# Performance work log

Measured on AMD Instinct MI355X. Metric: run time of the kernel, lower is better.

## Reference

```python
import jax, jax.numpy as jnp
import numpy as np

N_NODES = 100000
N_EDGES = 1600000
D_IN, D_HID, D_OUT = 256, 512, 48
K_STEPS = 10
ALPHA = 0.1


def setup_inputs() -> dict:
    key = jax.random.key(0)
    k_x, k_e, k_w1, k_w2 = jax.random.split(key, 4)
    x = jax.random.normal(k_x, (N_NODES, D_IN), dtype=jnp.float32)
    edge_index = jax.random.randint(k_e, (2, N_EDGES), 0, N_NODES, dtype=jnp.int64)
    # MLP params (Kaiming-ish scaling)
    W1 = jax.random.normal(k_w1, (D_IN, D_HID), dtype=jnp.float32) * (1.0 / np.sqrt(D_IN))
    b1 = jnp.zeros((D_HID,), dtype=jnp.float32)
    W2 = jax.random.normal(k_w2, (D_HID, D_OUT), dtype=jnp.float32) * (1.0 / np.sqrt(D_HID))
    b2 = jnp.zeros((D_OUT,), dtype=jnp.float32)
    return {"x": x, "edge_index": edge_index, "W1": W1, "b1": b1, "W2": W2, "b2": b2}


def reference(x, edge_index, W1, b1, W2, b2):
    N = x.shape[0]
    # --- MLP encoder ---
    h = jax.nn.relu(x @ W1 + b1) @ W2 + b2  # [N, D_OUT]

    # --- APPNP propagation (PyG defaults: add self-loops, symmetric gcn_norm) ---
    loop = jnp.arange(N, dtype=edge_index.dtype)
    src = jnp.concatenate([edge_index[0], loop])  # [E+N]
    dst = jnp.concatenate([edge_index[1], loop])
    ones = jnp.ones(src.shape[0], dtype=h.dtype)
    deg = jax.ops.segment_sum(ones, dst, num_segments=N)  # in-degree incl. self-loop
    dinv = jnp.where(deg > 0, jax.lax.rsqrt(deg), 0.0)
    norm = dinv[src] * dinv[dst]  # [E+N]

    out = h
    for _ in range(K_STEPS):
        msg = out[src] * norm[:, None]                      # gather + scale
        agg = jax.ops.segment_sum(msg, dst, num_segments=N)  # scatter-add
        out = (1.0 - ALPHA) * agg + ALPHA * h                # teleport mix
    return out
```

## Files before the change

kernel.cpp:

```cpp
#include <hip/hip_runtime.h>
#include <hip/hip_fp16.h>

constexpr int D_IN = 256, D_HID = 512, D_OUT = 48;
constexpr int HPAD = 64;
constexpr int K_STEPS = 10;

typedef __attribute__((ext_vector_type(8))) __bf16 bf16x8;
typedef __attribute__((ext_vector_type(4))) float f32x4;

__device__ __forceinline__ unsigned short f2bf(float f) {
  unsigned u = __builtin_bit_cast(unsigned, f);
  u += 0x7fffu + ((u >> 16) & 1u);
  return (unsigned short)(u >> 16);
}

__device__ __forceinline__ void gl2lds16(const unsigned short* g, unsigned short* l) {
  __builtin_amdgcn_global_load_lds(
      (const __attribute__((address_space(1))) unsigned int*)g,
      (__attribute__((address_space(3))) unsigned int*)l, 16, 0, 0);
}


__global__ void zero1_kernel(int* __restrict__ a, int N) {
  int i = blockIdx.x * 256 + threadIdx.x;
  if (i < N) a[i] = 0;
}

__global__ __launch_bounds__(256) void count_kernel(const int* __restrict__ dst,
                                                    int* __restrict__ cnt,
                                                    int* __restrict__ rank, int E) {
  int e = blockIdx.x * 256 + threadIdx.x;
  if (e >= E) return;
  int d = __builtin_nontemporal_load(dst + e);
  int r = atomicAdd(&cnt[d], 1);
  __builtin_nontemporal_store(r, rank + e);
}

__global__ void dinv_kernel(const int* __restrict__ cnt, float* __restrict__ dinv, int N) {
  int n = blockIdx.x * 256 + threadIdx.x;
  if (n < N) dinv[n] = rsqrtf((float)(cnt[n] + 1));
}

__global__ void scan1_kernel(const int* __restrict__ cnt, int* __restrict__ row_ptr,
                             int* __restrict__ bsum, int N) {
  __shared__ int sd[256];
  int tid = threadIdx.x, b = blockIdx.x;
  int i0 = b * 1024 + tid * 4;
  int v[4];
#pragma unroll
  for (int m = 0; m < 4; ++m) v[m] = (i0 + m < N) ? ((cnt[i0 + m] + 4) & ~3) : 0;
  int s = v[0] + v[1] + v[2] + v[3];
  sd[tid] = s;
  __syncthreads();
  for (int off = 1; off < 256; off <<= 1) {
    int t = (tid >= off) ? sd[tid - off] : 0;
    __syncthreads();
    sd[tid] += t;
    __syncthreads();
  }
  int run = sd[tid] - s;
#pragma unroll
  for (int m = 0; m < 4; ++m) {
    if (i0 + m < N) row_ptr[i0 + m] = run;
    run += v[m];
  }
  if (tid == 255) bsum[b] = sd[255];
}

__global__ void scan2_kernel(const int* __restrict__ bsum, int* __restrict__ bofs,
                             int* __restrict__ row_ptr, int NB, int N) {
  __shared__ int sd[128];
  int tid = threadIdx.x;
  int v = (tid < NB) ? bsum[tid] : 0;
  sd[tid] = v;
  __syncthreads();
  for (int off = 1; off < 128; off <<= 1) {
    int t = (tid >= off) ? sd[tid - off] : 0;
    __syncthreads();
    sd[tid] += t;
    __syncthreads();
  }
  if (tid < NB) bofs[tid] = sd[tid] - v;
  if (tid == 127) row_ptr[N] = sd[127];
}

__global__ void scan3_kernel(int* __restrict__ row_ptr, const int* __restrict__ bofs, int N) {
  int b = blockIdx.x;
  if (b == 0) return;
  int add = bofs[b];
  int i0 = b * 1024 + threadIdx.x * 4;
#pragma unroll
  for (int m = 0; m < 4; ++m)
    if (i0 + m < N) row_ptr[i0 + m] += add;
}

__global__ __launch_bounds__(256) void fill_kernel(
    const int* __restrict__ src, const int* __restrict__ dst,
    const int* __restrict__ row_ptr, const int* __restrict__ rank,
    int* __restrict__ edges, int E) {
  int e = blockIdx.x * 256 + threadIdx.x;
  if (e >= E) return;
  int d = __builtin_nontemporal_load(dst + e);
  int s = __builtin_nontemporal_load(src + e);
  int r = __builtin_nontemporal_load(rank + e);
  edges[row_ptr[d] + r] = s;
}

__global__ void pad_kernel(const int* __restrict__ cnt, const int* __restrict__ row_ptr,
                           int* __restrict__ edges, int N) {
  int n = blockIdx.x * 256 + threadIdx.x;
  if (n >= N) return;
  int a = row_ptr[n] + cnt[n];
  int b = row_ptr[n + 1];
  edges[a] = n;
  for (int p = a + 1; p < b; ++p) edges[p] = N;
}

__global__ void zrow_kernel(__half* __restrict__ a, __half* __restrict__ b, int N) {
  int t = threadIdx.x;
  a[(size_t)N * HPAD + t] = __float2half(0.f);
  b[(size_t)N * HPAD + t] = __float2half(0.f);
}


__global__ void convert_w1(const float* __restrict__ W1, unsigned short* __restrict__ W1F) {
  int i = blockIdx.x * 256 + threadIdx.x;
  if (i >= D_HID * D_IN) return;
  int c = i >> 8, k = i & 255;
  int ct = c >> 6, tn = (c >> 4) & 3, l15 = c & 15;
  int kb = k >> 5, q = (k >> 3) & 3, j = k & 7;
  int lane = (q << 4) | l15;
  int dst = (((ct * 4 + tn) * 8 + kb) << 9) + lane * 8 + j;
  W1F[dst] = f2bf(W1[k * D_HID + c]);
}

__global__ void convert_w2(const float* __restrict__ W2, unsigned short* __restrict__ W2F) {
  int i = blockIdx.x * 256 + threadIdx.x;
  if (i >= D_OUT * D_HID) return;
  int n = i >> 9, k = i & 511;
  int ct = k >> 6, kk = (k >> 5) & 1, q = (k >> 3) & 3, j = k & 7;
  int tn = n >> 4, l15 = n & 15;
  int lane = (q << 4) | l15;
  int dst = (((ct * 2 + kk) * 3 + tn) << 9) + lane * 8 + j;
  W2F[dst] = f2bf(W2[k * D_OUT + n]);
}


__global__ __launch_bounds__(512, 2) void encoder_kernel(
    const float* __restrict__ x, const float* __restrict__ b1,
    const float* __restrict__ b2, const float* __restrict__ dinvp,
    const unsigned short* __restrict__ W1F,
    const unsigned short* __restrict__ W2F,
    __half* __restrict__ h2, __half* __restrict__ qb, int N) {
  __shared__ unsigned short sW1[16384];
  __shared__ unsigned short sHid[8][16][72];
  __shared__ float sB1[512];
  __shared__ float sB2[64];

  int tid = threadIdx.x;
  int w = tid >> 6, lane = tid & 63;
  int q = lane >> 4, l15 = lane & 15;
  int row0 = blockIdx.x * 128 + w * 16;

  {
    const unsigned short* gsrc = W1F + (w << 9) + lane * 8;
    unsigned short* ldst = &sW1[w << 9];
#pragma unroll
    for (int i = 0; i < 4; ++i)
      gl2lds16(gsrc + (i << 12), ldst + (i << 12));
  }
  sB1[tid] = b1[tid];
  if (tid < 48) sB2[tid] = b2[tid];

  int grow = row0 + l15;
  bool rok = grow < N;
  const float* xr = x + (size_t)grow * D_IN;
  float4 xv[16];
#pragma unroll
  for (int jb = 0; jb < 8; ++jb) {
    xv[2 * jb]     = rok ? *(const float4*)(xr + jb * 32 + q * 8)
                         : make_float4(0.f, 0.f, 0.f, 0.f);
    xv[2 * jb + 1] = rok ? *(const float4*)(xr + jb * 32 + q * 8 + 4)
                         : make_float4(0.f, 0.f, 0.f, 0.f);
  }
  uint4 axu[8];
#pragma unroll
  for (int jb = 0; jb < 8; ++jb) {
    union { uint4 u; unsigned short s[8]; } uu;
    float4 v0 = xv[2 * jb], v1 = xv[2 * jb + 1];
    uu.s[0] = f2bf(v0.x); uu.s[1] = f2bf(v0.y); uu.s[2] = f2bf(v0.z); uu.s[3] = f2bf(v0.w);
    uu.s[4] = f2bf(v1.x); uu.s[5] = f2bf(v1.y); uu.s[6] = f2bf(v1.z); uu.s[7] = f2bf(v1.w);
    axu[jb] = uu.u;
  }

  f32x4 hacc[3];
#pragma unroll
  for (int t = 0; t < 3; ++t)
#pragma unroll
    for (int r = 0; r < 4; ++r) hacc[t][r] = 0.f;

  __syncthreads();

  for (int ct = 0; ct < 8; ++ct) {
    int c0 = ct * 64;
    f32x4 acc[4];
#pragma unroll
    for (int t = 0; t < 4; ++t)
#pragma unroll
      for (int r = 0; r < 4; ++r) acc[t][r] = 0.f;

    const unsigned short* sb = &sW1[lane * 8];
#pragma unroll
    for (int kb = 0; kb < 8; ++kb) {
      bf16x8 a = __builtin_bit_cast(bf16x8, axu[kb]);
      bf16x8 bq0 = *(const bf16x8*)(sb + (kb << 9));
      bf16x8 bq1 = *(const bf16x8*)(sb + (kb << 9) + 4096);
      bf16x8 bq2 = *(const bf16x8*)(sb + (kb << 9) + 8192);
      bf16x8 bq3 = *(const bf16x8*)(sb + (kb << 9) + 12288);
      acc[0] = __builtin_amdgcn_mfma_f32_16x16x32_bf16(a, bq0, acc[0], 0, 0, 0);
      acc[1] = __builtin_amdgcn_mfma_f32_16x16x32_bf16(a, bq1, acc[1], 0, 0, 0);
      acc[2] = __builtin_amdgcn_mfma_f32_16x16x32_bf16(a, bq2, acc[2], 0, 0, 0);
      acc[3] = __builtin_amdgcn_mfma_f32_16x16x32_bf16(a, bq3, acc[3], 0, 0, 0);
    }
#pragma unroll
    for (int tn = 0; tn < 4; ++tn) {
      int c = tn * 16 + l15;
      float bias = sB1[c0 + c];
#pragma unroll
      for (int rg = 0; rg < 4; ++rg) {
        float v = acc[tn][rg] + bias;
        v = v > 0.f ? v : 0.f;
        sHid[w][q * 4 + rg][c] = f2bf(v);
      }
    }
#pragma unroll
    for (int kk = 0; kk < 2; ++kk) {
      bf16x8 a0 = *(const bf16x8*)&sHid[w][l15][kk * 32 + q * 8];
      const unsigned short* w2b = W2F + (((ct * 2 + kk) * 3) << 9) + lane * 8;
#pragma unroll
      for (int tn = 0; tn < 3; ++tn) {
        bf16x8 b = *(const bf16x8*)(w2b + (tn << 9));
        hacc[tn] = __builtin_amdgcn_mfma_f32_16x16x32_bf16(a0, b, hacc[tn], 0, 0, 0);
      }
    }
    __syncthreads();
    if (ct < 7) {
      const unsigned short* gsrc = W1F + ((size_t)(ct + 1) << 14) + (w << 9) + lane * 8;
      unsigned short* ldst = &sW1[w << 9];
#pragma unroll
      for (int i = 0; i < 4; ++i)
        gl2lds16(gsrc + (i << 12), ldst + (i << 12));
      __syncthreads();
    }
  }
  float dv[4];
#pragma unroll
  for (int rg = 0; rg < 4; ++rg) {
    int gr = row0 + q * 4 + rg;
    dv[rg] = (gr < N) ? dinvp[gr] : 0.f;
  }
#pragma unroll
  for (int tn = 0; tn < 3; ++tn) {
    int c = tn * 16 + l15;
    float bias = sB2[c];
#pragma unroll
    for (int rg = 0; rg < 4; ++rg) {
      int gr = row0 + q * 4 + rg;
      if (gr < N) {
        float val = hacc[tn][rg] + bias;
        h2[(size_t)gr * HPAD + c] = __float2half(val);
        qb[(size_t)gr * HPAD + c] = __float2half(dv[rg] * val);
      }
    }
  }
#pragma unroll
  for (int rg = 0; rg < 4; ++rg) {
    int gr = row0 + q * 4 + rg;
    if (gr < N) {
      h2[(size_t)gr * HPAD + 48 + l15] = __float2half(0.f);
      qb[(size_t)gr * HPAD + 48 + l15] = __float2half(0.f);
    }
  }
}


__global__ __launch_bounds__(256) void prop_kernel(
    const __half* __restrict__ cur, const __half* __restrict__ h2,
    const float* __restrict__ dinv, const int* __restrict__ row_ptr,
    const int* __restrict__ edges, __half* __restrict__ nxt,
    float* __restrict__ outf, int N, int last) {
  int wid = (blockIdx.x * 256 + threadIdx.x) >> 6;
  int lane = threadIdx.x & 63;
  int half = lane >> 5;
  int slot = (lane >> 3) & 3;
  int s = lane & 7;
  int node = wid * 2 + half;
  bool nok = node < N;
  int p0 = 0, p1 = 0;
  if (nok) { int2 pp = *(const int2*)(row_ptr + node); p0 = pp.x; p1 = pp.y; }
  int d = p1 - p0;
  int dmax = max(d, __shfl_xor(d, 32));
  int nb = dmax >> 2;

  float acc[8];
#pragma unroll
  for (int i = 0; i < 8; ++i) acc[i] = 0.f;

  int p = p0 + slot;
  int e0 = N, e1 = N, e2 = N, e3 = N;
  if (nb > 0) e0 = edges[p];
  if (nb > 1) e1 = edges[p + 4];
  if (nb > 2) e2 = edges[p + 8];
  if (nb > 3) e3 = edges[p + 12];
  int b = 0;
  for (; b + 4 <= nb; b += 4) {
    int n0 = N, n1 = N, n2 = N, n3 = N;
    if (b + 4 < nb) n0 = edges[p + 16];
    if (b + 5 < nb) n1 = edges[p + 20];
    if (b + 6 < nb) n2 = edges[p + 24];
    if (b + 7 < nb) n3 = edges[p + 28];
    int i0 = (p      < p1) ? e0 : N;
    int i1 = (p + 4  < p1) ? e1 : N;
    int i2 = (p + 8  < p1) ? e2 : N;
    int i3 = (p + 12 < p1) ? e3 : N;
    union { float4 f; __half2 h[4]; } u0, u1, u2, u3;
    u0.f = *(const float4*)(cur + ((size_t)i0 << 6) + s * 8);
    u1.f = *(const float4*)(cur + ((size_t)i1 << 6) + s * 8);
    u2.f = *(const float4*)(cur + ((size_t)i2 << 6) + s * 8);
    u3.f = *(const float4*)(cur + ((size_t)i3 << 6) + s * 8);
#pragma unroll
    for (int i = 0; i < 4; ++i) {
      float2 f0 = __half22float2(u0.h[i]);
      float2 f1 = __half22float2(u1.h[i]);
      float2 f2 = __half22float2(u2.h[i]);
      float2 f3 = __half22float2(u3.h[i]);
      acc[2 * i]     += (f0.x + f1.x) + (f2.x + f3.x);
      acc[2 * i + 1] += (f0.y + f1.y) + (f2.y + f3.y);
    }
    e0 = n0; e1 = n1; e2 = n2; e3 = n3; p += 16;
  }
  if (b < nb) {
    int i0 = (p < p1) ? e0 : N;
    union { float4 f; __half2 h[4]; } u0;
    u0.f = *(const float4*)(cur + ((size_t)i0 << 6) + s * 8);
#pragma unroll
    for (int i = 0; i < 4; ++i) {
      float2 f0 = __half22float2(u0.h[i]);
      acc[2 * i]     += f0.x;
      acc[2 * i + 1] += f0.y;
    }
  }
  if (b + 1 < nb) {
    int i1 = (p + 4 < p1) ? e1 : N;
    union { float4 f; __half2 h[4]; } u1;
    u1.f = *(const float4*)(cur + ((size_t)i1 << 6) + s * 8);
#pragma unroll
    for (int i = 0; i < 4; ++i) {
      float2 f1 = __half22float2(u1.h[i]);
      acc[2 * i]     += f1.x;
      acc[2 * i + 1] += f1.y;
    }
  }
  if (b + 2 < nb) {
    int i2 = (p + 8 < p1) ? e2 : N;
    union { float4 f; __half2 h[4]; } u2;
    u2.f = *(const float4*)(cur + ((size_t)i2 << 6) + s * 8);
#pragma unroll
    for (int i = 0; i < 4; ++i) {
      float2 f2 = __half22float2(u2.h[i]);
      acc[2 * i]     += f2.x;
      acc[2 * i + 1] += f2.y;
    }
  }
#pragma unroll
  for (int i = 0; i < 8; ++i) {
    acc[i] += __int_as_float(__builtin_amdgcn_ds_swizzle(__float_as_int(acc[i]), 0x201F));
    acc[i] += __int_as_float(__builtin_amdgcn_ds_swizzle(__float_as_int(acc[i]), 0x401F));
  }
  if ((lane & 24) != 0 || !nok) return;
  float di = dinv[node];
  size_t base = ((size_t)node << 6) + s * 8;
  union { float4 f; __half2 h[4]; } uh;
  uh.f = *(const float4*)(h2 + base);
  float outv[8];
#pragma unroll
  for (int i = 0; i < 4; ++i) {
    float2 hf = __half22float2(uh.h[i]);
    outv[2 * i]     = 0.9f * di * acc[2 * i]     + 0.1f * hf.x;
    outv[2 * i + 1] = 0.9f * di * acc[2 * i + 1] + 0.1f * hf.y;
  }
  if (last) {
    if (s < 6) {
      float* op = outf + (size_t)node * D_OUT + s * 8;
      *(float4*)op       = make_float4(outv[0], outv[1], outv[2], outv[3]);
      *(float4*)(op + 4) = make_float4(outv[4], outv[5], outv[6], outv[7]);
    }
  } else {
    union { uint4 u4; __half2 h[4]; } o;
#pragma unroll
    for (int i = 0; i < 4; ++i)
      o.h[i] = __floats2half2_rn(di * outv[2 * i], di * outv[2 * i + 1]);
    *(uint4*)(nxt + base) = o.u4;
  }
}


extern "C" void kernel_launch(void* const* d_in, const int* in_sizes, int n_in,
                              void* d_out, int out_size, void* d_ws, size_t ws_size,
                              hipStream_t stream) {
  (void)n_in; (void)out_size; (void)ws_size;
  const float* x  = (const float*)d_in[0];
  const int*   ei = (const int*)d_in[1];
  const float* W1 = (const float*)d_in[2];
  const float* b1 = (const float*)d_in[3];
  const float* W2 = (const float*)d_in[4];
  const float* b2 = (const float*)d_in[5];
  const int N = in_sizes[0] / D_IN;
  const int E = in_sizes[1] / 2;
  const int* e_src = ei;
  const int* e_dst = ei + E;

  char* ws = (char*)d_ws;
  size_t off = 0;
  auto take = [&](size_t bytes) -> char* {
    char* p = ws + off;
    off += (bytes + 511) & ~(size_t)511;
    return p;
  };
  int* cnt      = (int*)take((size_t)N * 4);
  float* dinv   = (float*)take((size_t)N * 4);
  int* row_ptr  = (int*)take((size_t)(N + 1) * 4);
  int* bsum     = (int*)take(1024);
  int* bofs     = (int*)take(1024);
  int* rank     = (int*)take((size_t)E * 4);
  int* edges    = (int*)take(((size_t)E + 4 * (size_t)N + 2048) * 4);
  unsigned short* W1F = (unsigned short*)take((size_t)D_IN * D_HID * 2);
  unsigned short* W2F = (unsigned short*)take((size_t)D_HID * D_OUT * 2);
  __half* h2    = (__half*)take((size_t)N * HPAD * 2);
  __half* bufA  = (__half*)take((size_t)(N + 1) * HPAD * 2);
  __half* bufB  = (__half*)d_out;
  float* outp   = (float*)d_out;

  int nb256 = (N + 255) / 256;
  int eb256 = (E + 255) / 256;
  int NB    = (N + 1023) / 1024;

  zero1_kernel<<<nb256, 256, 0, stream>>>(cnt, N);
  count_kernel<<<eb256, 256, 0, stream>>>(e_dst, cnt, rank, E);
  dinv_kernel<<<nb256, 256, 0, stream>>>(cnt, dinv, N);
  scan1_kernel<<<NB, 256, 0, stream>>>(cnt, row_ptr, bsum, N);
  scan2_kernel<<<1, 128, 0, stream>>>(bsum, bofs, row_ptr, NB, N);
  scan3_kernel<<<NB, 256, 0, stream>>>(row_ptr, bofs, N);
  fill_kernel<<<eb256, 256, 0, stream>>>(e_src, e_dst, row_ptr, rank, edges, E);
  pad_kernel<<<nb256, 256, 0, stream>>>(cnt, row_ptr, edges, N);
  zrow_kernel<<<1, 64, 0, stream>>>(bufA, bufB, N);

  convert_w1<<<(D_IN * D_HID + 255) / 256, 256, 0, stream>>>(W1, W1F);
  convert_w2<<<(D_HID * D_OUT + 255) / 256, 256, 0, stream>>>(W2, W2F);
  encoder_kernel<<<(N + 127) / 128, 512, 0, stream>>>(x, b1, b2, dinv, W1F, W2F,
                                                      h2, bufB, N);

  int waves = (N + 1) / 2;
  int pblocks = (waves + 3) / 4;
  const __half* src = bufB;
  __half* dst = bufA;
  for (int it = 1; it <= K_STEPS; ++it) {
    int last = (it == K_STEPS);
    prop_kernel<<<pblocks, 256, 0, stream>>>(src, h2, dinv, row_ptr, edges,
                                             dst, outp, N, last);
    src = dst;
    dst = (dst == bufA) ? bufB : bufA;
  }
}
```

Measured before the change: 651.1 us.

## Partition edges by destination range before counting and CSR fill

```diff
diff --git a/kernel.cpp b/kernel.cpp
--- a/kernel.cpp
+++ b/kernel.cpp
@@ -21,19 +21,80 @@
 }
 
 
-__global__ void zero1_kernel(int* __restrict__ a, int N) {
+__global__ void zero2_kernel(int* __restrict__ a, int* __restrict__ b,
+                             int* __restrict__ cur, int N) {
   int i = blockIdx.x * 256 + threadIdx.x;
-  if (i < N) a[i] = 0;
-}
-
-__global__ __launch_bounds__(256) void count_kernel(const int* __restrict__ dst,
-                                                    int* __restrict__ cnt,
-                                                    int* __restrict__ rank, int E) {
-  int e = blockIdx.x * 256 + threadIdx.x;
-  if (e >= E) return;
-  int d = __builtin_nontemporal_load(dst + e);
-  int r = atomicAdd(&cnt[d], 1);
-  __builtin_nontemporal_store(r, rank + e);
+  if (i < N) { a[i] = 0; b[i] = 0; }
+  if (blockIdx.x == 0 && threadIdx.x < 128) cur[threadIdx.x] = 0;
+}
+
+__global__ __launch_bounds__(256) void part_kernel(
+    const int* __restrict__ src, const int* __restrict__ dst,
+    int2* __restrict__ fifo, int* __restrict__ cursor,
+    unsigned scale8, int CAP, int E) {
+  __shared__ int hcnt[8], hoff[8], hbase[8];
+  __shared__ int2 stage[256];
+  int tid = threadIdx.x;
+  int e = blockIdx.x * 256 + tid;
+  bool ok = e < E;
+  if (tid < 8) hcnt[tid] = 0;
+  __syncthreads();
+  int d = 0, s = 0, team = 0, local = 0;
+  if (ok) {
+    d = __builtin_nontemporal_load(dst + e);
+    s = __builtin_nontemporal_load(src + e);
+    team = (int)__umulhi((unsigned)d, scale8);
+    local = atomicAdd(&hcnt[team], 1);
+  }
+  __syncthreads();
+  if (tid == 0) {
+    int r = 0;
+#pragma unroll
+    for (int t = 0; t < 8; ++t) { hoff[t] = r; r += hcnt[t]; }
+  }
+  __syncthreads();
+  if (tid < 8 && hcnt[tid] > 0)
+    hbase[tid] = atomicAdd(&cursor[tid * 16], hcnt[tid]);
+  if (ok) stage[hoff[team] + local] = make_int2(s, d);
+  __syncthreads();
+  int total = min(256, E - blockIdx.x * 256);
+  if (tid < total) {
+    int t = 7;
+#pragma unroll
+    for (int k = 6; k >= 0; --k)
+      if (tid < hoff[k + 1]) t = k;
+    int2 v = stage[tid];
+    fifo[(size_t)t * CAP + hbase[t] + (tid - hoff[t])] = v;
+  }
+}
+
+__global__ __launch_bounds__(256) void count2_kernel(
+    const int2* __restrict__ fifo, const int* __restrict__ cursor,
+    int* __restrict__ cnt, int CAP) {
+  int t = blockIdx.x & 7;
+  int n = cursor[t * 16];
+  int stride = (gridDim.x >> 3) * 256;
+  for (int i = (blockIdx.x >> 3) * 256 + threadIdx.x; i < n; i += stride) {
+    long long v = __builtin_nontemporal_load((const long long*)fifo + (size_t)t * CAP + i);
+    int d = (int)(v >> 32);
+    atomicAdd(&cnt[d], 1);
+  }
+}
+
+__global__ __launch_bounds__(256) void fill2_kernel(
+    const int2* __restrict__ fifo, const int* __restrict__ cursor,
+    const int* __restrict__ row_ptr, int* __restrict__ cnt2,
+    int* __restrict__ edges, int CAP) {
+  int t = blockIdx.x & 7;
+  int n = cursor[t * 16];
+  int stride = (gridDim.x >> 3) * 256;
+  for (int i = (blockIdx.x >> 3) * 256 + threadIdx.x; i < n; i += stride) {
+    long long v = __builtin_nontemporal_load((const long long*)fifo + (size_t)t * CAP + i);
+    int s = (int)(v & 0xffffffffLL);
+    int d = (int)(v >> 32);
+    int r = atomicAdd(&cnt2[d], 1);
+    edges[row_ptr[d] + r] = s;
+  }
 }
 
 __global__ void dinv_kernel(const int* __restrict__ cnt, float* __restrict__ dinv, int N) {
@@ -92,18 +153,6 @@
 #pragma unroll
   for (int m = 0; m < 4; ++m)
     if (i0 + m < N) row_ptr[i0 + m] += add;
-}
-
-__global__ __launch_bounds__(256) void fill_kernel(
-    const int* __restrict__ src, const int* __restrict__ dst,
-    const int* __restrict__ row_ptr, const int* __restrict__ rank,
-    int* __restrict__ edges, int E) {
-  int e = blockIdx.x * 256 + threadIdx.x;
-  if (e >= E) return;
-  int d = __builtin_nontemporal_load(dst + e);
-  int s = __builtin_nontemporal_load(src + e);
-  int r = __builtin_nontemporal_load(rank + e);
-  edges[row_ptr[d] + r] = s;
 }
 
 __global__ void pad_kernel(const int* __restrict__ cnt, const int* __restrict__ row_ptr,
@@ -427,12 +476,15 @@
     off += (bytes + 511) & ~(size_t)511;
     return p;
   };
+  int CAP = E / 8 + E / 64 + 1024;
   int* cnt      = (int*)take((size_t)N * 4);
+  int* cnt2     = (int*)take((size_t)N * 4);
   float* dinv   = (float*)take((size_t)N * 4);
   int* row_ptr  = (int*)take((size_t)(N + 1) * 4);
   int* bsum     = (int*)take(1024);
   int* bofs     = (int*)take(1024);
-  int* rank     = (int*)take((size_t)E * 4);
+  int* cursor   = (int*)take(512);
+  int2* fifo    = (int2*)take((size_t)8 * CAP * 8);
   int* edges    = (int*)take(((size_t)E + 4 * (size_t)N + 2048) * 4);
   unsigned short* W1F = (unsigned short*)take((size_t)D_IN * D_HID * 2);
   unsigned short* W2F = (unsigned short*)take((size_t)D_HID * D_OUT * 2);
@@ -444,14 +496,16 @@
   int nb256 = (N + 255) / 256;
   int eb256 = (E + 255) / 256;
   int NB    = (N + 1023) / 1024;
-
-  zero1_kernel<<<nb256, 256, 0, stream>>>(cnt, N);
-  count_kernel<<<eb256, 256, 0, stream>>>(e_dst, cnt, rank, E);
+  unsigned scale8 = (unsigned)((8ULL << 32) / (unsigned long long)N);
+
+  zero2_kernel<<<nb256, 256, 0, stream>>>(cnt, cnt2, cursor, N);
+  part_kernel<<<eb256, 256, 0, stream>>>(e_src, e_dst, fifo, cursor, scale8, CAP, E);
+  count2_kernel<<<2048, 256, 0, stream>>>(fifo, cursor, cnt, CAP);
   dinv_kernel<<<nb256, 256, 0, stream>>>(cnt, dinv, N);
   scan1_kernel<<<NB, 256, 0, stream>>>(cnt, row_ptr, bsum, N);
   scan2_kernel<<<1, 128, 0, stream>>>(bsum, bofs, row_ptr, NB, N);
   scan3_kernel<<<NB, 256, 0, stream>>>(row_ptr, bofs, N);
-  fill_kernel<<<eb256, 256, 0, stream>>>(e_src, e_dst, row_ptr, rank, edges, E);
+  fill2_kernel<<<2048, 256, 0, stream>>>(fifo, cursor, row_ptr, cnt2, edges, CAP);
   pad_kernel<<<nb256, 256, 0, stream>>>(cnt, row_ptr, edges, N);
   zrow_kernel<<<1, 64, 0, stream>>>(bufA, bufB, N);
 
```

After: 797.0 us. 22.4% more time.
